# Kernel optimization log

Hardware: AMD Instinct MI355X
Metric: run time of the kernel (lower is better)

Reference implementation:

```python
import jax, jax.numpy as jnp
import numpy as np

B, M, N, HID, H, P = 16, 1024, 1024, 512, 8, 2
DH = HID // H


def setup_inputs() -> dict:
    key = jax.random.key(0)
    k1, k2, k3, k4 = jax.random.split(key, 4)
    X = jax.random.normal(k1, (B, M, HID), dtype=jnp.float32)
    Y = jax.random.normal(k2, (B, N, HID), dtype=jnp.float32)
    # learned pad prefixes (kaiming-uniform in torch; any init is fine for a numerics baseline)
    bound = np.sqrt(1.0 / HID)
    pad_x = jax.random.uniform(k3, (P, HID), dtype=jnp.float32, minval=-bound, maxval=bound)
    pad_y = jax.random.uniform(k4, (P, HID), dtype=jnp.float32, minval=-bound, maxval=bound)
    return {"X": X, "Y": Y, "pad_x": pad_x, "pad_y": pad_y}


def _project(T, pad):
    # prepend learned pad rows, split into heads -> [B, H, L+P, DH]
    b = T.shape[0]
    T = jnp.concatenate([jnp.broadcast_to(pad[None], (b, P, HID)), T], axis=1)
    return T.reshape(b, T.shape[1], H, DH).transpose(0, 2, 1, 3)


def reference(X, Y, pad_x, pad_y):
    Xp = _project(X, pad_x)  # [B,H,Mp,DH], query=key=value
    Yp = _project(Y, pad_y)  # [B,H,Np,DH]
    # shared similarity matrix (no 1/sqrt(d) scaling in the original)
    sim = jnp.einsum('bhmd,bhnd->bhmn', Xp, Yp)  # [B,H,Mp,Np]
    # masks in the original are all-ones (pad rows + torch.ones), so masked_fill is a no-op
    attn_X_by_Y = jax.nn.softmax(sim, axis=2)  # softmax over Mp (rows)
    attn_Y_by_X = jax.nn.softmax(sim, axis=3)  # softmax over Np (cols)
    # X attends in Y: attn^T @ X_value -> [B,H,Np,DH]
    X_in_Y = jnp.einsum('bhmn,bhmd->bhnd', attn_X_by_Y, Xp)[:, :, P:, :]
    X_in_Y = X_in_Y.transpose(0, 2, 1, 3).reshape(X.shape[0], -1, HID)  # [B,N,HID]
    # Y attends in X: attn @ Y_value -> [B,H,Mp,DH]
    Y_in_X = jnp.einsum('bhmn,bhnd->bhmd', attn_Y_by_X, Yp)[:, :, P:, :]
    Y_in_X = Y_in_X.transpose(0, 2, 1, 3).reshape(Y.shape[0], -1, HID)  # [B,M,HID]
    return X_in_Y, Y_in_X
```

## Files before the change

kernel.cpp:

```cpp
#include <hip/hip_runtime.h>
#include <hip/hip_bf16.h>
#include <stdint.h>

typedef _Float16 f16x8_t  __attribute__((ext_vector_type(8)));
typedef float    f32x16_t __attribute__((ext_vector_type(16)));
typedef short    s16x8_t  __attribute__((ext_vector_type(8)));
typedef unsigned uint2v   __attribute__((ext_vector_type(2)));
typedef unsigned int u32;

#define MFMA32 __builtin_amdgcn_mfma_f32_32x32x16_f16

#if __has_builtin(__builtin_amdgcn_exp2f)
#define EXP2(x) __builtin_amdgcn_exp2f(x)
#else
#define EXP2(x) exp2f(x)
#endif

__device__ __forceinline__ u32 PKRTZ(float a, float b) {
    return __builtin_bit_cast(u32, __builtin_amdgcn_cvt_pkrtz(a, b));
}

__device__ __forceinline__ void PLSWAP(u32& a, u32& b) {
#if __has_builtin(__builtin_amdgcn_permlane32_swap)
    uint2v r = __builtin_amdgcn_permlane32_swap(a, b, false, false);
    a = r[0]; b = r[1];
#else
    u32 pa = (u32)__shfl_xor((int)a, 32);
    u32 pb = (u32)__shfl_xor((int)b, 32);
    const int hi_ = (int)((threadIdx.x & 63) >> 5);
    u32 na = hi_ ? pb : a;
    u32 nb = hi_ ? b  : pa;
    a = na; b = nb;
#endif
}
__device__ __forceinline__ float swap_add(float v) {
    u32 a = __builtin_bit_cast(u32, v), b = a;
    PLSWAP(a, b);
    return __builtin_bit_cast(float, a) + __builtin_bit_cast(float, b);
}
__device__ __forceinline__ float swap_max(float v) {
    u32 a = __builtin_bit_cast(u32, v), b = a;
    PLSWAP(a, b);
    return fmaxf(__builtin_bit_cast(float, a), __builtin_bit_cast(float, b));
}

constexpr int Bb   = 16;
constexpr int HIDc = 512;
constexpr int SEQc = 1024;

constexpr int QT = 128;
constexpr int KT = 64;
constexpr int NTILES = SEQc / KT;

constexpr float LOG2E_F = 1.4426950408889634f;
constexpr float DTHR    = 11.5f;

constexpr int ROWB       = 144;
constexpr int VT_OFF     = 64 * ROWB;
constexpr int BUF_STRIDE = 2 * VT_OFF;
constexpr int LDS_TOTAL  = 2 * BUF_STRIDE;

__global__ __launch_bounds__(256, 4)
void xattn_kernel(const float* __restrict__ X, const float* __restrict__ Y,
                  const float* __restrict__ padx, const float* __restrict__ pady,
                  float* __restrict__ out)
{
    __shared__ __align__(16) unsigned char pool[LDS_TOTAL];

    const int tid  = threadIdx.x;
    const int w    = tid >> 6;
    const int lane = tid & 63;
    const int l31  = lane & 31;
    const int hi   = lane >> 5;

    const unsigned hid = blockIdx.x + gridDim.x * (blockIdx.y + gridDim.y * blockIdx.z);
    const unsigned lid = (hid & 7u) * 256u + (hid >> 3);
    const int qt   = lid & 7;
    const int bh   = (lid >> 3) & 127;
    const int pass = lid >> 10;
    const int b    = bh >> 3;
    const int h    = bh & 7;

    const float* Qp   = pass == 0 ? X : Y;
    const float* KVp  = pass == 0 ? Y : X;
    const float* padp = pass == 0 ? pady : padx;
    float* outp = out + (pass == 0 ? (size_t)Bb * SEQc * HIDc : (size_t)0);

    const float* qrow = Qp + ((size_t)b * SEQc + qt * QT + w * 32 + l31) * HIDc + h * 64;
    f16x8_t qf[4];
#pragma unroll
    for (int ds = 0; ds < 4; ++ds) {
        const float* src = qrow + ds * 16 + hi * 8;
        float4 a = *(const float4*)src;
        float4 c = *(const float4*)(src + 4);
        uint4 uu = {PKRTZ(a.x * LOG2E_F, a.y * LOG2E_F), PKRTZ(a.z * LOG2E_F, a.w * LOG2E_F),
                    PKRTZ(c.x * LOG2E_F, c.y * LOG2E_F), PKRTZ(c.z * LOG2E_F, c.w * LOG2E_F)};
        qf[ds] = __builtin_bit_cast(f16x8_t, uu);
    }

    const float* padh = padp + h * 64;
    float s0 = 0.f, s1 = 0.f;
#pragma unroll
    for (int ds = 0; ds < 4; ++ds)
#pragma unroll
        for (int j = 0; j < 8; ++j) {
            float qv = (float)qf[ds][j];
            int d = ds * 16 + hi * 8 + j;
            s0 += qv * padh[d];
            s1 += qv * padh[HIDc + d];
        }
    s0 = swap_add(s0);
    s1 = swap_add(s1);
    float mr = fmaxf(s0, s1);
    float e0 = EXP2(s0 - mr), e1 = EXP2(s1 - mr);
    float lr  = e0 + e1;
    float lrp = 0.f;

    f32x16_t Oacc[2];
#pragma unroll
    for (int db = 0; db < 2; ++db)
#pragma unroll
        for (int r = 0; r < 16; ++r) {
            int d = db * 32 + (r & 3) + 8 * (r >> 2) + 4 * hi;
            Oacc[db][r] = e0 * padh[d] + e1 * padh[HIDc + d];
        }

    const unsigned kkey = (unsigned)(((l31 >> 3) & 3) << 4);
    const unsigned vkey = (unsigned)((l31 >> 3) << 4);
    const unsigned rowb = (unsigned)(l31 * ROWB);
    unsigned kcol[4], vcol[4];
#pragma unroll
    for (int s = 0; s < 4; ++s) {
        kcol[s] = (unsigned)((s * 32 + hi * 16) ^ kkey);
        vcol[s] = (unsigned)(VT_OFF + ((s * 32 + hi * 16) ^ vkey));
    }

    const int tr = tid >> 3, tc = tid & 7;
    const float* ksrc = KVp + ((size_t)b * SEQc + 2 * tr) * HIDc + h * 64 + tc * 8;
    const unsigned kw  = (unsigned)((2 * tr) * ROWB + ((tc * 16) ^ ((((2 * tr) >> 3) & 3) << 4)));
    const unsigned vtw = (unsigned)(VT_OFF + (tc * 8) * ROWB + ((4 * tr) ^ (tc << 4)));

    auto loadtile = [&](int idx, float4& a0, float4& a1, float4& c0, float4& c1) {
        const float* srow = ksrc + (size_t)idx * KT * HIDc;
        a0 = *(const float4*)srow;          a1 = *(const float4*)(srow + 4);
        c0 = *(const float4*)(srow + HIDc); c1 = *(const float4*)(srow + HIDc + 4);
    };
    auto stage_write = [&](int bo, const float4& a0, const float4& a1,
                           const float4& c0, const float4& c1) {
        uint4 k0 = {PKRTZ(a0.x, a0.y), PKRTZ(a0.z, a0.w), PKRTZ(a1.x, a1.y), PKRTZ(a1.z, a1.w)};
        uint4 k1 = {PKRTZ(c0.x, c0.y), PKRTZ(c0.z, c0.w), PKRTZ(c1.x, c1.y), PKRTZ(c1.z, c1.w)};
        *(uint4*)(pool + bo + kw) = k0;
        *(uint4*)(pool + bo + kw + ROWB) = k1;
        float fa[8] = {a0.x, a0.y, a0.z, a0.w, a1.x, a1.y, a1.z, a1.w};
        float fc[8] = {c0.x, c0.y, c0.z, c0.w, c1.x, c1.y, c1.z, c1.w};
#pragma unroll
        for (int j = 0; j < 8; ++j)
            *(u32*)(pool + bo + vtw + j * ROWB) = PKRTZ(fa[j], fc[j]);
    };

    auto compute = [&](int bo) {
        f32x16_t sa[2];
#pragma unroll
        for (int nb = 0; nb < 2; ++nb)
#pragma unroll
            for (int r = 0; r < 16; ++r) sa[nb][r] = 0.f;
        __builtin_amdgcn_s_setprio(1);
#pragma unroll
        for (int ds = 0; ds < 4; ++ds) {
            s16x8_t k0 = *(const s16x8_t*)(pool + bo + rowb + kcol[ds]);
            s16x8_t k1 = *(const s16x8_t*)(pool + bo + rowb + kcol[ds] + 32 * ROWB);
            sa[0] = MFMA32(__builtin_bit_cast(f16x8_t, k0), qf[ds], sa[0], 0, 0, 0);
            sa[1] = MFMA32(__builtin_bit_cast(f16x8_t, k1), qf[ds], sa[1], 0, 0, 0);
        }
        __builtin_amdgcn_s_setprio(0);

        float m16[16];
#pragma unroll
        for (int i = 0; i < 16; ++i) m16[i] = fmaxf(sa[0][i], sa[1][i]);
        float m8[8];
#pragma unroll
        for (int i = 0; i < 8; ++i) m8[i] = fmaxf(m16[2 * i], m16[2 * i + 1]);
        float m4[4];
#pragma unroll
        for (int i = 0; i < 4; ++i) m4[i] = fmaxf(m8[2 * i], m8[2 * i + 1]);
        float pm = fmaxf(fmaxf(m4[0], m4[1]), fmaxf(m4[2], m4[3]));
        pm = swap_max(pm);
        if (!__all(pm <= mr + DTHR)) {
            float mn = fmaxf(mr, pm);
            float corr = EXP2(mr - mn);
            mr = mn;
            lr  *= corr;
            lrp *= corr;
#pragma unroll
            for (int db = 0; db < 2; ++db)
#pragma unroll
                for (int r = 0; r < 16; ++r) Oacc[db][r] *= corr;
        }

        float ps = 0.f;
        __builtin_amdgcn_s_setprio(1);
#pragma unroll
        for (int nb = 0; nb < 2; ++nb)
#pragma unroll
            for (int ksl = 0; ksl < 2; ++ksl) {
                float x0 = EXP2(sa[nb][8 * ksl + 0] - mr);
                float x1 = EXP2(sa[nb][8 * ksl + 1] - mr);
                float x2 = EXP2(sa[nb][8 * ksl + 2] - mr);
                float x3 = EXP2(sa[nb][8 * ksl + 3] - mr);
                float x4 = EXP2(sa[nb][8 * ksl + 4] - mr);
                float x5 = EXP2(sa[nb][8 * ksl + 5] - mr);
                float x6 = EXP2(sa[nb][8 * ksl + 6] - mr);
                float x7 = EXP2(sa[nb][8 * ksl + 7] - mr);
                ps += ((x0 + x1) + (x2 + x3)) + ((x4 + x5) + (x6 + x7));
                u32 w0 = PKRTZ(x0, x1);
                u32 w1 = PKRTZ(x2, x3);
                u32 w2 = PKRTZ(x4, x5);
                u32 w3 = PKRTZ(x6, x7);
                PLSWAP(w0, w2);
                PLSWAP(w1, w3);
                uint4 pu = {w0, w1, w2, w3};
                f16x8_t pfrag = __builtin_bit_cast(f16x8_t, pu);
                const int ks = nb * 2 + ksl;
                s16x8_t v0 = *(const s16x8_t*)(pool + bo + rowb + vcol[ks]);
                s16x8_t v1 = *(const s16x8_t*)(pool + bo + rowb + (vcol[ks] ^ 0x40u) + 32 * ROWB);
                Oacc[0] = MFMA32(__builtin_bit_cast(f16x8_t, v0), pfrag, Oacc[0], 0, 0, 0);
                Oacc[1] = MFMA32(__builtin_bit_cast(f16x8_t, v1), pfrag, Oacc[1], 0, 0, 0);
            }
        __builtin_amdgcn_s_setprio(0);
        lrp += ps;
    };

    {
        float4 a0, a1, c0, c1;
        loadtile(0, a0, a1, c0, c1);
        stage_write(0, a0, a1, c0, c1);
    }
    __syncthreads();
    for (int kt = 0; kt < NTILES; kt += 2) {
        {
            float4 a0, a1, c0, c1;
            loadtile(kt + 1, a0, a1, c0, c1);
            compute(0);
            stage_write(BUF_STRIDE, a0, a1, c0, c1);
            __syncthreads();
        }
        {
            float4 a0, a1, c0, c1;
            const bool more = (kt + 2 < NTILES);
            if (more) loadtile(kt + 2, a0, a1, c0, c1);
            compute(BUF_STRIDE);
            if (more) stage_write(0, a0, a1, c0, c1);
            __syncthreads();
        }
    }

    const float lfull = lr + swap_add(lrp);
    {
        const float inv = 1.0f / lfull;
        float* fp = (float*)pool;
#pragma unroll
        for (int db = 0; db < 2; ++db)
#pragma unroll
            for (int r = 0; r < 16; ++r) {
                int d = db * 32 + (r & 3) + 8 * (r >> 2) + 4 * hi;
                fp[(w * 32 + l31) * 68 + d] = Oacc[db][r] * inv;
            }
    }
    __syncthreads();
    {
        const int row = tid >> 1, ch = tid & 1;
        const float* srcp = (const float*)pool + row * 68 + ch * 32;
        float* dst = outp + ((size_t)b * SEQc + qt * QT + row) * HIDc + h * 64 + ch * 32;
#pragma unroll
        for (int k = 0; k < 8; ++k)
            *(float4*)(dst + k * 4) = *(const float4*)(srcp + k * 4);
    }
}

extern "C" void kernel_launch(void* const* d_in, const int* in_sizes, int n_in,
                              void* d_out, int out_size, void* d_ws, size_t ws_size,
                              hipStream_t stream) {
    const float* X    = (const float*)d_in[0];
    const float* Y    = (const float*)d_in[1];
    const float* padx = (const float*)d_in[2];
    const float* pady = (const float*)d_in[3];
    float* out = (float*)d_out;
    (void)in_sizes; (void)n_in; (void)out_size; (void)d_ws; (void)ws_size;

    dim3 grid(SEQc / QT, Bb * 8, 2);
    hipLaunchKernelGGL(xattn_kernel, grid, dim3(256), 0, stream, X, Y, padx, pady, out);
}
```

Measured before the change: 116.5 us.

## Software-pipeline QK and softmax-PV across triple-buffered 32-key tiles

Halves the key tile to 32 rows and adds a third LDS buffer. Each step now computes QK for one tile while the softmax and PV for the previous tile overlap the staging of the next one, with two global loads kept in flight. The K/V LDS layout loses its XOR swizzle and V gets a narrower row pitch. Occupancy drops from 4 to 3 blocks per CU, and the new layout risks LDS bank conflicts and needs more syncs per key.

```diff
diff --git a/kernel.cpp b/kernel.cpp
--- a/kernel.cpp
+++ b/kernel.cpp
@@ -49,18 +49,20 @@
 constexpr int SEQc = 1024;
 
 constexpr int QT = 128;
-constexpr int KT = 64;
-constexpr int NTILES = SEQc / KT;
+constexpr int KT = 32;
+constexpr int NT = SEQc / KT;
 
 constexpr float LOG2E_F = 1.4426950408889634f;
 constexpr float DTHR    = 11.5f;
 
-constexpr int ROWB       = 144;
-constexpr int VT_OFF     = 64 * ROWB;
-constexpr int BUF_STRIDE = 2 * VT_OFF;
-constexpr int LDS_TOTAL  = 2 * BUF_STRIDE;
-
-__global__ __launch_bounds__(256, 4)
+constexpr int KROWB  = 144;
+constexpr int VROWB  = 80;
+constexpr int VT_OFF = KT * KROWB;
+constexpr int BUFB   = VT_OFF + 64 * VROWB;
+constexpr int B0 = 0, B1 = BUFB, B2 = 2 * BUFB;
+constexpr int LDS_TOTAL = 34816;
+
+__global__ __launch_bounds__(256, 3)
 void xattn_kernel(const float* __restrict__ X, const float* __restrict__ Y,
                   const float* __restrict__ padx, const float* __restrict__ pady,
                   float* __restrict__ out)
@@ -125,65 +127,46 @@
             Oacc[db][r] = e0 * padh[d] + e1 * padh[HIDc + d];
         }
 
-    const unsigned kkey = (unsigned)(((l31 >> 3) & 3) << 4);
-    const unsigned vkey = (unsigned)((l31 >> 3) << 4);
-    const unsigned rowb = (unsigned)(l31 * ROWB);
-    unsigned kcol[4], vcol[4];
-#pragma unroll
-    for (int s = 0; s < 4; ++s) {
-        kcol[s] = (unsigned)((s * 32 + hi * 16) ^ kkey);
-        vcol[s] = (unsigned)(VT_OFF + ((s * 32 + hi * 16) ^ vkey));
-    }
-
-    const int tr = tid >> 3, tc = tid & 7;
-    const float* ksrc = KVp + ((size_t)b * SEQc + 2 * tr) * HIDc + h * 64 + tc * 8;
-    const unsigned kw  = (unsigned)((2 * tr) * ROWB + ((tc * 16) ^ ((((2 * tr) >> 3) & 3) << 4)));
-    const unsigned vtw = (unsigned)(VT_OFF + (tc * 8) * ROWB + ((4 * tr) ^ (tc << 4)));
-
-    auto loadtile = [&](int idx, float4& a0, float4& a1, float4& c0, float4& c1) {
-        const float* srow = ksrc + (size_t)idx * KT * HIDc;
-        a0 = *(const float4*)srow;          a1 = *(const float4*)(srow + 4);
-        c0 = *(const float4*)(srow + HIDc); c1 = *(const float4*)(srow + HIDc + 4);
+    const unsigned kbase = (unsigned)(l31 * KROWB + hi * 16);
+    const unsigned vbase = (unsigned)(VT_OFF + l31 * VROWB + hi * 16);
+
+    const int tr = tid >> 4, tc2 = tid & 15;
+    const float* ksrc = KVp + ((size_t)b * SEQc + 2 * tr) * HIDc + h * 64 + tc2 * 4;
+    const unsigned kwb  = (unsigned)((2 * tr) * KROWB + tc2 * 8);
+    const unsigned vtwb = (unsigned)(VT_OFF + (tc2 * 4) * VROWB + tr * 4);
+
+    auto stage = [&](int bo, const float4& va, const float4& vb) {
+        uint2 k0 = {PKRTZ(va.x, va.y), PKRTZ(va.z, va.w)};
+        uint2 k1 = {PKRTZ(vb.x, vb.y), PKRTZ(vb.z, vb.w)};
+        *(uint2*)(pool + bo + kwb) = k0;
+        *(uint2*)(pool + bo + kwb + KROWB) = k1;
+        float fa[4] = {va.x, va.y, va.z, va.w};
+        float fb[4] = {vb.x, vb.y, vb.z, vb.w};
+#pragma unroll
+        for (int j = 0; j < 4; ++j)
+            *(u32*)(pool + bo + vtwb + j * VROWB) = PKRTZ(fa[j], fb[j]);
     };
-    auto stage_write = [&](int bo, const float4& a0, const float4& a1,
-                           const float4& c0, const float4& c1) {
-        uint4 k0 = {PKRTZ(a0.x, a0.y), PKRTZ(a0.z, a0.w), PKRTZ(a1.x, a1.y), PKRTZ(a1.z, a1.w)};
-        uint4 k1 = {PKRTZ(c0.x, c0.y), PKRTZ(c0.z, c0.w), PKRTZ(c1.x, c1.y), PKRTZ(c1.z, c1.w)};
-        *(uint4*)(pool + bo + kw) = k0;
-        *(uint4*)(pool + bo + kw + ROWB) = k1;
-        float fa[8] = {a0.x, a0.y, a0.z, a0.w, a1.x, a1.y, a1.z, a1.w};
-        float fc[8] = {c0.x, c0.y, c0.z, c0.w, c1.x, c1.y, c1.z, c1.w};
-#pragma unroll
-        for (int j = 0; j < 8; ++j)
-            *(u32*)(pool + bo + vtw + j * ROWB) = PKRTZ(fa[j], fc[j]);
+
+    auto qk = [&](f32x16_t& sa, int bo) {
+#pragma unroll
+        for (int r = 0; r < 16; ++r) sa[r] = 0.f;
+        __builtin_amdgcn_s_setprio(1);
+#pragma unroll
+        for (int ds = 0; ds < 4; ++ds) {
+            s16x8_t k0 = *(const s16x8_t*)(pool + bo + kbase + ds * 32);
+            sa = MFMA32(__builtin_bit_cast(f16x8_t, k0), qf[ds], sa, 0, 0, 0);
+        }
+        __builtin_amdgcn_s_setprio(0);
     };
 
-    auto compute = [&](int bo) {
-        f32x16_t sa[2];
-#pragma unroll
-        for (int nb = 0; nb < 2; ++nb)
-#pragma unroll
-            for (int r = 0; r < 16; ++r) sa[nb][r] = 0.f;
-        __builtin_amdgcn_s_setprio(1);
-#pragma unroll
-        for (int ds = 0; ds < 4; ++ds) {
-            s16x8_t k0 = *(const s16x8_t*)(pool + bo + rowb + kcol[ds]);
-            s16x8_t k1 = *(const s16x8_t*)(pool + bo + rowb + kcol[ds] + 32 * ROWB);
-            sa[0] = MFMA32(__builtin_bit_cast(f16x8_t, k0), qf[ds], sa[0], 0, 0, 0);
-            sa[1] = MFMA32(__builtin_bit_cast(f16x8_t, k1), qf[ds], sa[1], 0, 0, 0);
-        }
-        __builtin_amdgcn_s_setprio(0);
-
-        float m16[16];
-#pragma unroll
-        for (int i = 0; i < 16; ++i) m16[i] = fmaxf(sa[0][i], sa[1][i]);
-        float m8[8];
-#pragma unroll
-        for (int i = 0; i < 8; ++i) m8[i] = fmaxf(m16[2 * i], m16[2 * i + 1]);
-        float m4[4];
-#pragma unroll
-        for (int i = 0; i < 4; ++i) m4[i] = fmaxf(m8[2 * i], m8[2 * i + 1]);
-        float pm = fmaxf(fmaxf(m4[0], m4[1]), fmaxf(m4[2], m4[3]));
+    auto smpv = [&](f32x16_t& sa, int bo) {
+        float p0 = fmaxf(sa[0], sa[1]),   p1 = fmaxf(sa[2], sa[3]);
+        float p2 = fmaxf(sa[4], sa[5]),   p3 = fmaxf(sa[6], sa[7]);
+        p0 = fmaxf(p0, fmaxf(sa[8], sa[9]));
+        p1 = fmaxf(p1, fmaxf(sa[10], sa[11]));
+        p2 = fmaxf(p2, fmaxf(sa[12], sa[13]));
+        p3 = fmaxf(p3, fmaxf(sa[14], sa[15]));
+        float pm = fmaxf(fmaxf(p0, p1), fmaxf(p2, p3));
         pm = swap_max(pm);
         if (!__all(pm <= mr + DTHR)) {
             float mn = fmaxf(mr, pm);
@@ -196,65 +179,74 @@
 #pragma unroll
                 for (int r = 0; r < 16; ++r) Oacc[db][r] *= corr;
         }
-
         float ps = 0.f;
         __builtin_amdgcn_s_setprio(1);
 #pragma unroll
-        for (int nb = 0; nb < 2; ++nb)
-#pragma unroll
-            for (int ksl = 0; ksl < 2; ++ksl) {
-                float x0 = EXP2(sa[nb][8 * ksl + 0] - mr);
-                float x1 = EXP2(sa[nb][8 * ksl + 1] - mr);
-                float x2 = EXP2(sa[nb][8 * ksl + 2] - mr);
-                float x3 = EXP2(sa[nb][8 * ksl + 3] - mr);
-                float x4 = EXP2(sa[nb][8 * ksl + 4] - mr);
-                float x5 = EXP2(sa[nb][8 * ksl + 5] - mr);
-                float x6 = EXP2(sa[nb][8 * ksl + 6] - mr);
-                float x7 = EXP2(sa[nb][8 * ksl + 7] - mr);
-                ps += ((x0 + x1) + (x2 + x3)) + ((x4 + x5) + (x6 + x7));
-                u32 w0 = PKRTZ(x0, x1);
-                u32 w1 = PKRTZ(x2, x3);
-                u32 w2 = PKRTZ(x4, x5);
-                u32 w3 = PKRTZ(x6, x7);
-                PLSWAP(w0, w2);
-                PLSWAP(w1, w3);
-                uint4 pu = {w0, w1, w2, w3};
-                f16x8_t pfrag = __builtin_bit_cast(f16x8_t, pu);
-                const int ks = nb * 2 + ksl;
-                s16x8_t v0 = *(const s16x8_t*)(pool + bo + rowb + vcol[ks]);
-                s16x8_t v1 = *(const s16x8_t*)(pool + bo + rowb + (vcol[ks] ^ 0x40u) + 32 * ROWB);
-                Oacc[0] = MFMA32(__builtin_bit_cast(f16x8_t, v0), pfrag, Oacc[0], 0, 0, 0);
-                Oacc[1] = MFMA32(__builtin_bit_cast(f16x8_t, v1), pfrag, Oacc[1], 0, 0, 0);
-            }
+        for (int ks = 0; ks < 2; ++ks) {
+            float x0 = EXP2(sa[8 * ks + 0] - mr);
+            float x1 = EXP2(sa[8 * ks + 1] - mr);
+            float x2 = EXP2(sa[8 * ks + 2] - mr);
+            float x3 = EXP2(sa[8 * ks + 3] - mr);
+            float x4 = EXP2(sa[8 * ks + 4] - mr);
+            float x5 = EXP2(sa[8 * ks + 5] - mr);
+            float x6 = EXP2(sa[8 * ks + 6] - mr);
+            float x7 = EXP2(sa[8 * ks + 7] - mr);
+            ps += ((x0 + x1) + (x2 + x3)) + ((x4 + x5) + (x6 + x7));
+            u32 w0 = PKRTZ(x0, x1);
+            u32 w1 = PKRTZ(x2, x3);
+            u32 w2 = PKRTZ(x4, x5);
+            u32 w3 = PKRTZ(x6, x7);
+            PLSWAP(w0, w2);
+            PLSWAP(w1, w3);
+            uint4 pu = {w0, w1, w2, w3};
+            f16x8_t pfrag = __builtin_bit_cast(f16x8_t, pu);
+            s16x8_t v0 = *(const s16x8_t*)(pool + bo + vbase + ks * 32);
+            s16x8_t v1 = *(const s16x8_t*)(pool + bo + vbase + ks * 32 + 32 * VROWB);
+            Oacc[0] = MFMA32(__builtin_bit_cast(f16x8_t, v0), pfrag, Oacc[0], 0, 0, 0);
+            Oacc[1] = MFMA32(__builtin_bit_cast(f16x8_t, v1), pfrag, Oacc[1], 0, 0, 0);
+        }
         __builtin_amdgcn_s_setprio(0);
         lrp += ps;
     };
 
-    {
-        float4 a0, a1, c0, c1;
-        loadtile(0, a0, a1, c0, c1);
-        stage_write(0, a0, a1, c0, c1);
-    }
-    __syncthreads();
-    for (int kt = 0; kt < NTILES; kt += 2) {
-        {
-            float4 a0, a1, c0, c1;
-            loadtile(kt + 1, a0, a1, c0, c1);
-            compute(0);
-            stage_write(BUF_STRIDE, a0, a1, c0, c1);
-            __syncthreads();
-        }
-        {
-            float4 a0, a1, c0, c1;
-            const bool more = (kt + 2 < NTILES);
-            if (more) loadtile(kt + 2, a0, a1, c0, c1);
-            compute(BUF_STRIDE);
-            if (more) stage_write(0, a0, a1, c0, c1);
-            __syncthreads();
-        }
-    }
+    float4 s0a, s0b, s1a, s1b;
+    f32x16_t sa0, sa1;
+#define LOADSET(Sa, Sb, T) { const float* srow_ = ksrc + (size_t)(T) * KT * HIDc; \
+        Sa = *(const float4*)srow_; Sb = *(const float4*)(srow_ + HIDc); }
+#define STEP(T, SAF, SAD, BQ, BS, BD, LA, LB, SA_, SB_)  \
+    {                                                     \
+        if ((T) + 2 < NT) LOADSET(LA, LB, (T) + 2);       \
+        qk(SAF, BQ);                                      \
+        stage(BS, SA_, SB_);                              \
+        smpv(SAD, BD);                                    \
+        __syncthreads();                                  \
+    }
+
+    LOADSET(s0a, s0b, 0);
+    stage(B0, s0a, s0b);
+    LOADSET(s1a, s1b, 1);
+    __syncthreads();
+    qk(sa0, B0);
+    stage(B1, s1a, s1b);
+    LOADSET(s0a, s0b, 2);
+    __syncthreads();
+
+    for (int t0 = 1; t0 + 5 <= 30; t0 += 6) {
+        STEP(t0 + 0, sa1, sa0, B1, B2, B0, s1a, s1b, s0a, s0b)
+        STEP(t0 + 1, sa0, sa1, B2, B0, B1, s0a, s0b, s1a, s1b)
+        STEP(t0 + 2, sa1, sa0, B0, B1, B2, s1a, s1b, s0a, s0b)
+        STEP(t0 + 3, sa0, sa1, B1, B2, B0, s0a, s0b, s1a, s1b)
+        STEP(t0 + 4, sa1, sa0, B2, B0, B1, s1a, s1b, s0a, s0b)
+        STEP(t0 + 5, sa0, sa1, B0, B1, B2, s0a, s0b, s1a, s1b)
+    }
+    qk(sa1, B1);
+    smpv(sa0, B0);
+    smpv(sa1, B1);
+#undef LOADSET
+#undef STEP
 
     const float lfull = lr + swap_add(lrp);
+    __syncthreads();
     {
         const float inv = 1.0f / lfull;
         float* fp = (float*)pool;
```

Measured after the change: 114.7 us. No clear change (-1.5%).
